# Kernel tuning notes

Measured on AMD Instinct MI355X. Metric: run time of the kernel, lower is better.

The kernel has to match this reference:

```python
import jax, jax.numpy as jnp
import numpy as np

N = 32768      # total nodes
E = 262144     # total edges
B = 32         # graphs in batch
NP = N // B    # nodes per graph (equal-sized graphs)
K = 820        # ceil(0.8 * NP), PyG TopKPooling k
H, C = 8, 64   # heads, per-head channels
NEG_SLOPE = 0.2


def setup_inputs() -> dict:
    key = jax.random.key(0)
    ks = jax.random.split(key, 12)
    s = 0.05
    return {
        "x": jax.random.normal(ks[0], (N, 256), jnp.float32),
        "edge_attr": jax.random.normal(ks[1], (E, 32), jnp.float32),
        "Wl": jax.random.normal(ks[2], (256, H * C), jnp.float32) * s,
        "bl": jax.random.normal(ks[3], (H * C,), jnp.float32) * s,
        "Wr": jax.random.normal(ks[4], (256, H * C), jnp.float32) * s,
        "br": jax.random.normal(ks[5], (H * C,), jnp.float32) * s,
        "We": jax.random.normal(ks[6], (32, H * C), jnp.float32) * s,
        "att": jax.random.normal(ks[7], (H, C), jnp.float32) * s,
        "bias": jax.random.normal(ks[8], (H * C,), jnp.float32) * s,
        "pool_w": jax.random.normal(ks[9], (H * C,), jnp.float32),
        "edge_index": jax.random.randint(ks[10], (2, E), 0, N, jnp.int32),
    }


def reference(x, edge_attr, Wl, bl, Wr, br, We, att, bias, pool_w, edge_index):
    src, dst = edge_index[0], edge_index[1]
    # GATv2Conv (eval mode, dropout off)
    xl = (x @ Wl + bl).reshape(N, H, C)   # x_j side (lin_l)
    xr = (x @ Wr + br).reshape(N, H, C)   # x_i side (lin_r)
    e = (edge_attr @ We).reshape(E, H, C)  # lin_edge, bias=False
    m = jax.nn.leaky_relu(xl[src] + xr[dst] + e, NEG_SLOPE)   # [E,H,C]
    alpha = jnp.einsum('ehc,hc->eh', m, att)                  # [E,H]
    amax = jax.ops.segment_max(alpha, dst, num_segments=N)
    ex = jnp.exp(alpha - amax[dst])
    denom = jax.ops.segment_sum(ex, dst, num_segments=N)
    alpha = ex / denom[dst]                                   # segment softmax over dst
    out = jax.ops.segment_sum(alpha[..., None] * xl[src], dst, num_segments=N)
    h = jax.nn.relu(out.reshape(N, H * C) + bias)             # [N,512]
    # TopKPooling: score = tanh(x.w / ||w||), keep top-k per graph, scale kept rows
    score = jnp.tanh(h @ pool_w / jnp.sqrt(jnp.sum(pool_w * pool_w)))
    vals, idx = jax.lax.top_k(score.reshape(B, NP), K)        # [B,K]
    hg = h.reshape(B, NP, H * C)
    hsel = jnp.take_along_axis(hg, idx[..., None], axis=1) * vals[..., None]  # [B,K,512]
    # global max pool || global mean pool
    gmp = hsel.max(axis=1)
    gap = hsel.mean(axis=1)
    return jnp.concatenate([gmp, gap], axis=1)                # [B,1024]
```

## Files before the change

### kernel.cpp

```cpp
#include <hip/hip_runtime.h>
#include <hip/hip_bf16.h>
#include <cstdint>
#include <cstddef>

#define N_NODES 32768
#define N_EDGES 262144
#define BGRAPH  32
#define NPG     1024
#define KSEL    820
#define NEG     0.2f

typedef unsigned short u16;
typedef __attribute__((ext_vector_type(4))) float f32x4;
typedef __attribute__((ext_vector_type(8))) short s16x8;

static __device__ __forceinline__ u16 f2bf(float v) {
    __hip_bfloat16 b(v);
    return *reinterpret_cast<u16*>(&b);
}
static __device__ __forceinline__ float bf2f(u16 u) {
    __hip_bfloat16 b = *reinterpret_cast<__hip_bfloat16*>(&u);
    return (float)b;
}

__global__ __launch_bounds__(256) void k_split_x(
    const float* __restrict__ x, u16* __restrict__ xhi, u16* __restrict__ xlo)
{
    const int i = blockIdx.x * 256 + threadIdx.x;
    const float4 v = *(const float4*)&x[(size_t)i * 4];
    u16 h0 = f2bf(v.x), h1 = f2bf(v.y), h2 = f2bf(v.z), h3 = f2bf(v.w);
    u16 l0 = f2bf(v.x - bf2f(h0));
    u16 l1 = f2bf(v.y - bf2f(h1));
    u16 l2 = f2bf(v.z - bf2f(h2));
    u16 l3 = f2bf(v.w - bf2f(h3));
    *(ushort4*)&xhi[(size_t)i * 4] = make_ushort4(h0, h1, h2, h3);
    *(ushort4*)&xlo[(size_t)i * 4] = make_ushort4(l0, l1, l2, l3);
}

__global__ __launch_bounds__(256) void k_pack_bt(
    const float* __restrict__ Wl, const float* __restrict__ Wr,
    u16* __restrict__ BpT)
{
    const int kp = blockIdx.x * 256 + threadIdx.x;
    const int n  = blockIdx.y;
    if (kp >= 768) return;
    const float* W = (n < 512) ? Wl : Wr;
    const int col = n & 511;
    const int k = kp & 255;
    const float v = W[(size_t)k * 512 + col];
    const u16 h = f2bf(v);
    const u16 o = (kp >= 256 && kp < 512) ? f2bf(v - bf2f(h)) : h;
    BpT[(size_t)n * 768 + kp] = o;
}

__global__ __launch_bounds__(256) void gemm_mfma(
    const u16* __restrict__ xhi, const u16* __restrict__ xlo,
    const u16* __restrict__ BpT,
    const float* __restrict__ bl, const float* __restrict__ br,
    float* __restrict__ xl, float* __restrict__ xr)
{
    __shared__ u16 As[128 * 64];
    __shared__ u16 Bs[128 * 64];

    const int raw = blockIdx.x;
    const int swz = (raw & 7) * 256 + (raw >> 3);
    const int mt = swz & 255, nt = swz >> 8;
    const int m0 = mt * 128, n0 = nt * 128;

    const int tid  = threadIdx.x;
    const int lane = tid & 63;
    const int wid  = tid >> 6;
    const int wr   = wid >> 1, wc = wid & 1;
    const int lr   = lane & 15;
    const int lk   = lane >> 4;

    f32x4 acc[4][4] = {};

    for (int tk = 0; tk < 12; ++tk) {
        const u16* asrc = (tk < 8) ? xhi : xlo;
        const int  kcol = (tk & 3) * 64;
        __syncthreads();
#pragma unroll
        for (int p = 0; p < 4; ++p) {
            const int c   = tid + p * 256;
            const int row = c >> 3;
            const int ko  = (c & 7) * 8;
            const int di  = row * 64 + (ko ^ ((row & 7) << 3));
            *(uint4*)&As[di] = *(const uint4*)&asrc[(size_t)(m0 + row) * 256 + kcol + ko];
            *(uint4*)&Bs[di] = *(const uint4*)&BpT[(size_t)(n0 + row) * 768 + tk * 64 + ko];
        }
        __syncthreads();
#pragma unroll
        for (int kk = 0; kk < 2; ++kk) {
            s16x8 af[4], bfr[4];
            const int akw = kk * 32 + lk * 8;
#pragma unroll
            for (int i = 0; i < 4; ++i) {
                const int arow = wr * 64 + i * 16 + lr;
                af[i]  = *(const s16x8*)&As[arow * 64 + (akw ^ ((arow & 7) << 3))];
                const int brow = wc * 64 + i * 16 + lr;
                bfr[i] = *(const s16x8*)&Bs[brow * 64 + (akw ^ ((brow & 7) << 3))];
            }
#pragma unroll
            for (int i = 0; i < 4; ++i)
#pragma unroll
                for (int j = 0; j < 4; ++j)
                    acc[i][j] = __builtin_amdgcn_mfma_f32_16x16x32_bf16(
                        af[i], bfr[j], acc[i][j], 0, 0, 0);
        }
    }

    float* const outp = (n0 < 512) ? xl : xr;
    const int ocol0 = n0 & 511;
    const float* const bb = (n0 < 512) ? bl : br;
#pragma unroll
    for (int j = 0; j < 4; ++j) {
        const int col = ocol0 + wc * 64 + j * 16 + lr;
        const float bv = bb[col];
#pragma unroll
        for (int i = 0; i < 4; ++i) {
#pragma unroll
            for (int r = 0; r < 4; ++r) {
                const int rowg = m0 + wr * 64 + i * 16 + (lane >> 4) * 4 + r;
                outp[(size_t)rowg * 512 + col] = acc[i][j][r] + bv;
            }
        }
    }
}

__global__ void k_hist(const int* __restrict__ ei, int* __restrict__ counts)
{
    int e = blockIdx.x * 256 + threadIdx.x;
    if (e < N_EDGES) atomicAdd(&counts[ei[N_EDGES + e]], 1);
}

__global__ __launch_bounds__(1024) void k_scan(
    const int* __restrict__ counts, int* __restrict__ offsets, int* __restrict__ cursors)
{
    __shared__ int part[1024];
    const int tid = threadIdx.x;
    const int base = tid * 32;
    int loc[32];
    int s = 0;
#pragma unroll
    for (int i = 0; i < 32; ++i) { loc[i] = s; s += counts[base + i]; }
    part[tid] = s;
    __syncthreads();
    const int own = s;
    for (int off = 1; off < 1024; off <<= 1) {
        int v = (tid >= off) ? part[tid - off] : 0;
        __syncthreads();
        part[tid] += v;
        __syncthreads();
    }
    const int pre = part[tid] - own;
#pragma unroll
    for (int i = 0; i < 32; ++i) {
        int o = pre + loc[i];
        offsets[base + i] = o;
        cursors[base + i] = o;
    }
}

__global__ void k_scatter(const int* __restrict__ ei, int* __restrict__ cursors,
                          int* __restrict__ sorted_src, int* __restrict__ sorted_dst,
                          int* __restrict__ sorted_eid)
{
    int e = blockIdx.x * 256 + threadIdx.x;
    if (e >= N_EDGES) return;
    int d = ei[N_EDGES + e];
    int pos = atomicAdd(&cursors[d], 1);
    sorted_src[pos] = ei[e];
    sorted_dst[pos] = d;
    sorted_eid[pos] = e;
}

#define EPB 32

__global__ __launch_bounds__(256, 4) void k_alpha(
    const float* __restrict__ xl, const float* __restrict__ xr,
    const float* __restrict__ ea, const float* __restrict__ We,
    const float* __restrict__ att,
    const int* __restrict__ sorted_src, const int* __restrict__ sorted_dst,
    const int* __restrict__ sorted_eid,
    float* __restrict__ logits)
{
    const int tid = threadIdx.x;
    const int c0 = tid * 2;
    const int head = tid >> 5;
    const int lead = ((tid & 31) == 0);

    float2 wr[32];
#pragma unroll
    for (int k = 0; k < 32; ++k)
        wr[k] = *(const float2*)&We[k * 512 + c0];
#pragma unroll
    for (int k = 0; k < 32; ++k)
        asm volatile("" : "+v"(wr[k].x), "+v"(wr[k].y));
    const float2 attv = *(const float2*)&att[c0];

    const int p0 = blockIdx.x * EPB;
    for (int j = 0; j < EPB; j += 2) {
        const int pA = p0 + j, pB = p0 + j + 1;
        const int sA = sorted_src[pA], sB = sorted_src[pB];
        const int dA = sorted_dst[pA], dB = sorted_dst[pB];
        const int eA = sorted_eid[pA], eB = sorted_eid[pB];
        const float2 xlA = *(const float2*)&xl[(size_t)sA * 512 + c0];
        const float2 xrA = *(const float2*)&xr[(size_t)dA * 512 + c0];
        const float2 xlB = *(const float2*)&xl[(size_t)sB * 512 + c0];
        const float2 xrB = *(const float2*)&xr[(size_t)dB * 512 + c0];
        const float* eaA = &ea[(size_t)eA * 32];
        const float* eaB = &ea[(size_t)eB * 32];

        float a0 = 0.f, a1 = 0.f, b0 = 0.f, b1 = 0.f;
#pragma unroll
        for (int k = 0; k < 32; ++k) {
            const float evA = eaA[k];
            const float evB = eaB[k];
            a0 += evA * wr[k].x; a1 += evA * wr[k].y;
            b0 += evB * wr[k].x; b1 += evB * wr[k].y;
        }
        float tA0 = xlA.x + xrA.x + a0; tA0 = tA0 > 0.f ? tA0 : NEG * tA0;
        float tA1 = xlA.y + xrA.y + a1; tA1 = tA1 > 0.f ? tA1 : NEG * tA1;
        float tB0 = xlB.x + xrB.x + b0; tB0 = tB0 > 0.f ? tB0 : NEG * tB0;
        float tB1 = xlB.y + xrB.y + b1; tB1 = tB1 > 0.f ? tB1 : NEG * tB1;

        float lA = tA0 * attv.x + tA1 * attv.y;
        float lB = tB0 * attv.x + tB1 * attv.y;
#pragma unroll
        for (int o = 1; o < 32; o <<= 1) {
            lA += __shfl_xor(lA, o);
            lB += __shfl_xor(lB, o);
        }
        if (lead) {
            logits[(size_t)pA * 8 + head] = lA;
            logits[(size_t)pB * 8 + head] = lB;
        }
    }
}

#define AGG_DPB 8

__global__ __launch_bounds__(256, 8) void k_agg(
    const float* __restrict__ xl, const float* __restrict__ logits,
    const int* __restrict__ sorted_src,
    const int* __restrict__ offsets, const int* __restrict__ counts,
    const float* __restrict__ bias, const float* __restrict__ pw,
    float* __restrict__ h, float* __restrict__ score)
{
    __shared__ float red_s[4];

    const int tid = threadIdx.x;
    const int wv  = tid >> 6;
    const int l   = tid & 63;
    const int c0  = tid * 2;
    const int head = tid >> 5;

    const float2 bv  = *(const float2*)&bias[c0];
    const float2 pwv = *(const float2*)&pw[c0];

    float nrm = pwv.x * pwv.x + pwv.y * pwv.y;
#pragma unroll
    for (int o = 1; o < 64; o <<= 1) nrm += __shfl_xor(nrm, o);
    if (l == 0) red_s[wv] = nrm;
    __syncthreads();
    const float inv_nrm = 1.0f / sqrtf(red_s[0] + red_s[1] + red_s[2] + red_s[3]);

    for (int dd = 0; dd < AGG_DPB; ++dd) {
        const int d   = blockIdx.x * AGG_DPB + dd;
        const int off = offsets[d];
        const int deg = counts[d];

        float m = -INFINITY;
        for (int j = 0; j < deg; ++j)
            m = fmaxf(m, logits[(size_t)(off + j) * 8 + head]);

        float den = 0.f, a0 = 0.f, a1 = 0.f;
        for (int j = 0; j < deg; ++j) {
            const float lg = logits[(size_t)(off + j) * 8 + head];
            const int   s  = sorted_src[off + j];
            const float2 xl2 = *(const float2*)&xl[(size_t)s * 512 + c0];
            const float pe = __expf(lg - m);
            den += pe;
            a0 += pe * xl2.x;
            a1 += pe * xl2.y;
        }

        const float r = den > 0.f ? 1.0f / den : 0.f;
        const float h0 = fmaxf(a0 * r + bv.x, 0.f);
        const float h1 = fmaxf(a1 * r + bv.y, 0.f);
        *(float2*)&h[(size_t)d * 512 + c0] = make_float2(h0, h1);

        float ps = h0 * pwv.x + h1 * pwv.y;
#pragma unroll
        for (int o = 1; o < 64; o <<= 1) ps += __shfl_xor(ps, o);
        __syncthreads();
        if (l == 0) red_s[wv] = ps;
        __syncthreads();
        if (tid == 0)
            score[d] = tanhf((red_s[0] + red_s[1] + red_s[2] + red_s[3]) * inv_nrm);
    }
}

__global__ __launch_bounds__(256) void k_topk(const float* __restrict__ score,
                                              int* __restrict__ sel_idx,
                                              float* __restrict__ sel_val)
{
    __shared__ unsigned long long key[1024];
    const int g = blockIdx.x, tid = threadIdx.x;
    for (int i = tid; i < 1024; i += 256) {
        float s = score[g * 1024 + i];
        unsigned u = __float_as_uint(s);
        u = (u & 0x80000000u) ? ~u : (u | 0x80000000u);
        key[i] = ((unsigned long long)(~u) << 32) | (unsigned)i;
    }
    __syncthreads();
    for (int k = 2; k <= 1024; k <<= 1) {
        for (int j = k >> 1; j > 0; j >>= 1) {
            for (int i = tid; i < 1024; i += 256) {
                int ixj = i ^ j;
                if (ixj > i) {
                    bool up = ((i & k) == 0);
                    unsigned long long a = key[i], b = key[ixj];
                    if ((a > b) == up) { key[i] = b; key[ixj] = a; }
                }
            }
            __syncthreads();
        }
    }
    for (int kk = tid; kk < KSEL; kk += 256) {
        int idx = (int)(key[kk] & 0xFFFFFFFFu);
        sel_idx[g * KSEL + kk] = idx;
        sel_val[g * KSEL + kk] = score[g * 1024 + idx];
    }
}

#define KSLICE 103

__global__ __launch_bounds__(256) void k_pool_part(
    const float* __restrict__ h, const int* __restrict__ sel_idx,
    const float* __restrict__ sel_val, float* __restrict__ part)
{
    const int g = blockIdx.x >> 3, sl = blockIdx.x & 7;
    const int kbeg = sl * KSLICE;
    const int kend = min(KSEL, kbeg + KSLICE);
    const int n = kend - kbeg;
    __shared__ float vs[KSLICE];
    __shared__ int   is_[KSLICE];
    const int tid = threadIdx.x;
    if (tid < n) {
        vs[tid]  = sel_val[g * KSEL + kbeg + tid];
        is_[tid] = sel_idx[g * KSEL + kbeg + tid];
    }
    __syncthreads();
    const int c0 = tid, c1 = tid + 256;
    float mx0 = -INFINITY, mx1 = -INFINITY, s0 = 0.f, s1 = 0.f;
    for (int kk = 0; kk < n; ++kk) {
        const float* hp = h + ((size_t)(g * 1024 + is_[kk])) * 512;
        const float v = vs[kk];
        float f0 = hp[c0] * v, f1 = hp[c1] * v;
        mx0 = fmaxf(mx0, f0); s0 += f0;
        mx1 = fmaxf(mx1, f1); s1 += f1;
    }
    const size_t base = ((size_t)blockIdx.x * 2) * 512;
    part[base + c0] = mx0;        part[base + c1] = mx1;
    part[base + 512 + c0] = s0;   part[base + 512 + c1] = s1;
}

__global__ __launch_bounds__(256) void k_pool_merge(
    const float* __restrict__ part, float* __restrict__ out)
{
    const int g = blockIdx.x, tid = threadIdx.x;
    const int c0 = tid, c1 = tid + 256;
    float mx0 = -INFINITY, mx1 = -INFINITY, s0 = 0.f, s1 = 0.f;
    for (int sl = 0; sl < 8; ++sl) {
        const size_t base = ((size_t)(g * 8 + sl) * 2) * 512;
        mx0 = fmaxf(mx0, part[base + c0]); mx1 = fmaxf(mx1, part[base + c1]);
        s0 += part[base + 512 + c0];       s1 += part[base + 512 + c1];
    }
    out[(size_t)g * 1024 + c0] = mx0;
    out[(size_t)g * 1024 + c1] = mx1;
    out[(size_t)g * 1024 + 512 + c0] = s0 * (1.f / KSEL);
    out[(size_t)g * 1024 + 512 + c1] = s1 * (1.f / KSEL);
}

extern "C" void kernel_launch(void* const* d_in, const int* in_sizes, int n_in,
                              void* d_out, int out_size, void* d_ws, size_t ws_size,
                              hipStream_t stream)
{
    const float* x    = (const float*)d_in[0];
    const float* ea   = (const float*)d_in[1];
    const float* Wl   = (const float*)d_in[2];
    const float* bl   = (const float*)d_in[3];
    const float* Wr   = (const float*)d_in[4];
    const float* br   = (const float*)d_in[5];
    const float* We   = (const float*)d_in[6];
    const float* att  = (const float*)d_in[7];
    const float* bias = (const float*)d_in[8];
    const float* pw   = (const float*)d_in[9];
    const int*   ei   = (const int*)d_in[10];
    float* out = (float*)d_out;

    float* xl        = (float*)d_ws;
    float* xr        = xl + (size_t)N_NODES * 512;
    float* h         = xr + (size_t)N_NODES * 512;
    float* logits    = h + (size_t)N_NODES * 512;
    float* sel_val   = logits + (size_t)N_EDGES * 8;
    float* part      = sel_val + BGRAPH * KSEL;
    float* score     = part + 256 * 2 * 512;
    int* counts      = (int*)(score + N_NODES);
    int* offsets     = counts + N_NODES;
    int* cursors     = offsets + N_NODES;
    int* sorted_src  = cursors + N_NODES;
    int* sorted_dst  = sorted_src + N_EDGES;
    int* sorted_eid  = sorted_dst + N_EDGES;
    int* sel_idx     = sorted_eid + N_EDGES;
    u16* xhi         = (u16*)(sel_idx + BGRAPH * KSEL);
    u16* xlo         = xhi + (size_t)N_NODES * 256;
    u16* bpt         = xlo + (size_t)N_NODES * 256;

    hipMemsetAsync(counts, 0, (size_t)N_NODES * sizeof(int), stream);

    k_split_x<<<(N_NODES * 256) / (4 * 256), 256, 0, stream>>>(x, xhi, xlo);
    k_pack_bt<<<dim3(3, 1024), 256, 0, stream>>>(Wl, Wr, bpt);
    gemm_mfma<<<2048, 256, 0, stream>>>(xhi, xlo, bpt, bl, br, xl, xr);

    k_hist<<<N_EDGES / 256, 256, 0, stream>>>(ei, counts);
    k_scan<<<1, 1024, 0, stream>>>(counts, offsets, cursors);
    k_scatter<<<N_EDGES / 256, 256, 0, stream>>>(ei, cursors, sorted_src, sorted_dst, sorted_eid);
    k_alpha<<<N_EDGES / EPB, 256, 0, stream>>>(xl, xr, ea, We, att,
                                               sorted_src, sorted_dst, sorted_eid, logits);
    k_agg<<<N_NODES / AGG_DPB, 256, 0, stream>>>(xl, logits, sorted_src, offsets, counts,
                                                 bias, pw, h, score);
    k_topk<<<BGRAPH, 256, 0, stream>>>(score, sel_idx, sel_val);
    k_pool_part<<<BGRAPH * 8, 256, 0, stream>>>(h, sel_idx, sel_val, part);
    k_pool_merge<<<BGRAPH, 256, 0, stream>>>(part, out);
}
```

Measured before the change: 679.7 us.

## Compute edge logits with split-bf16 MFMA and use direct global-to-LDS loads in GEMM

The edge-logit kernel is rewritten to compute the edge_attr @ We projection on MFMA units with hi/lo bf16 splitting (three-term product), tiling 64 edges per step and splitting the 512 channels across 4 column slabs in grid.y. The leaky-relu and attention dot product are then fused per slab and reduced with shuffles. Separately, the main GEMM's tile loads now use global_load_lds to write straight into LDS with a pre-swizzled source column, bypassing registers. Risks: slab splitting re-gathers xl/xr rows with less coalescing (16-float runs), and the hi/lo approximation changes precision slightly.

```diff
diff --git a/kernel.cpp b/kernel.cpp
--- a/kernel.cpp
+++ b/kernel.cpp
@@ -21,6 +21,12 @@
 static __device__ __forceinline__ float bf2f(u16 u) {
     __hip_bfloat16 b = *reinterpret_cast<__hip_bfloat16*>(&u);
     return (float)b;
+}
+
+typedef const __attribute__((address_space(1))) void* gas_p;
+typedef __attribute__((address_space(3))) void* las_p;
+static __device__ __forceinline__ void gload16(const void* g, void* l) {
+    __builtin_amdgcn_global_load_lds((gas_p)g, (las_p)l, 16, 0, 0);
 }
 
 __global__ __launch_bounds__(256) void k_split_x(
@@ -82,12 +88,13 @@
         __syncthreads();
 #pragma unroll
         for (int p = 0; p < 4; ++p) {
-            const int c   = tid + p * 256;
+            const int c   = p * 256 + wid * 64 + lane;
             const int row = c >> 3;
-            const int ko  = (c & 7) * 8;
-            const int di  = row * 64 + (ko ^ ((row & 7) << 3));
-            *(uint4*)&As[di] = *(const uint4*)&asrc[(size_t)(m0 + row) * 256 + kcol + ko];
-            *(uint4*)&Bs[di] = *(const uint4*)&BpT[(size_t)(n0 + row) * 768 + tk * 64 + ko];
+            const int cs  = ((c & 7) ^ (row & 7)) * 8;
+            gload16(&asrc[(size_t)(m0 + row) * 256 + kcol + cs],
+                    &As[(size_t)(p * 256 + wid * 64) * 8]);
+            gload16(&BpT[(size_t)(n0 + row) * 768 + tk * 64 + cs],
+                    &Bs[(size_t)(p * 256 + wid * 64) * 8]);
         }
         __syncthreads();
 #pragma unroll
@@ -175,9 +182,9 @@
     sorted_eid[pos] = e;
 }
 
-#define EPB 32
-
-__global__ __launch_bounds__(256, 4) void k_alpha(
+#define LT_TILES 8
+
+__global__ __launch_bounds__(256, 4) void k_logit(
     const float* __restrict__ xl, const float* __restrict__ xr,
     const float* __restrict__ ea, const float* __restrict__ We,
     const float* __restrict__ att,
@@ -185,56 +192,89 @@
     const int* __restrict__ sorted_eid,
     float* __restrict__ logits)
 {
-    const int tid = threadIdx.x;
-    const int c0 = tid * 2;
-    const int head = tid >> 5;
-    const int lead = ((tid & 31) == 0);
-
-    float2 wr[32];
-#pragma unroll
-    for (int k = 0; k < 32; ++k)
-        wr[k] = *(const float2*)&We[k * 512 + c0];
-#pragma unroll
-    for (int k = 0; k < 32; ++k)
-        asm volatile("" : "+v"(wr[k].x), "+v"(wr[k].y));
-    const float2 attv = *(const float2*)&att[c0];
-
-    const int p0 = blockIdx.x * EPB;
-    for (int j = 0; j < EPB; j += 2) {
-        const int pA = p0 + j, pB = p0 + j + 1;
-        const int sA = sorted_src[pA], sB = sorted_src[pB];
-        const int dA = sorted_dst[pA], dB = sorted_dst[pB];
-        const int eA = sorted_eid[pA], eB = sorted_eid[pB];
-        const float2 xlA = *(const float2*)&xl[(size_t)sA * 512 + c0];
-        const float2 xrA = *(const float2*)&xr[(size_t)dA * 512 + c0];
-        const float2 xlB = *(const float2*)&xl[(size_t)sB * 512 + c0];
-        const float2 xrB = *(const float2*)&xr[(size_t)dB * 512 + c0];
-        const float* eaA = &ea[(size_t)eA * 32];
-        const float* eaB = &ea[(size_t)eB * 32];
-
-        float a0 = 0.f, a1 = 0.f, b0 = 0.f, b1 = 0.f;
-#pragma unroll
-        for (int k = 0; k < 32; ++k) {
-            const float evA = eaA[k];
-            const float evB = eaB[k];
-            a0 += evA * wr[k].x; a1 += evA * wr[k].y;
-            b0 += evB * wr[k].x; b1 += evB * wr[k].y;
-        }
-        float tA0 = xlA.x + xrA.x + a0; tA0 = tA0 > 0.f ? tA0 : NEG * tA0;
-        float tA1 = xlA.y + xrA.y + a1; tA1 = tA1 > 0.f ? tA1 : NEG * tA1;
-        float tB0 = xlB.x + xrB.x + b0; tB0 = tB0 > 0.f ? tB0 : NEG * tB0;
-        float tB1 = xlB.y + xrB.y + b1; tB1 = tB1 > 0.f ? tB1 : NEG * tB1;
-
-        float lA = tA0 * attv.x + tA1 * attv.y;
-        float lB = tB0 * attv.x + tB1 * attv.y;
-#pragma unroll
-        for (int o = 1; o < 32; o <<= 1) {
-            lA += __shfl_xor(lA, o);
-            lB += __shfl_xor(lB, o);
-        }
-        if (lead) {
-            logits[(size_t)pA * 8 + head] = lA;
-            logits[(size_t)pB * 8 + head] = lB;
+    __shared__ u16 Ws[128 * 104];
+    __shared__ u16 Ae[64 * 104];
+    __shared__ int eid_s[64], src_s[64], dst_s[64];
+
+    const int tid  = threadIdx.x;
+    const int lane = tid & 63;
+    const int wid  = tid >> 6;
+    const int slab = blockIdx.y;
+    const int lr   = lane & 15;
+    const int lk   = lane >> 4;
+
+    for (int idx = tid; idx < 128 * 96; idx += 256) {
+        const int ch = idx / 96, kp = idx % 96;
+        const int k = (kp < 32) ? kp : ((kp < 64) ? kp - 32 : kp - 64);
+        const float v = We[(size_t)k * 512 + slab * 128 + ch];
+        const u16 h = f2bf(v);
+        Ws[ch * 104 + kp] = (kp >= 64) ? f2bf(v - bf2f(h)) : h;
+    }
+    float attw[8];
+#pragma unroll
+    for (int f = 0; f < 8; ++f) attw[f] = att[slab * 128 + f * 16 + lr];
+
+    for (int t = 0; t < LT_TILES; ++t) {
+        const int ebase = (blockIdx.x * LT_TILES + t) * 64;
+        __syncthreads();
+        if (tid < 64) {
+            eid_s[tid] = sorted_eid[ebase + tid];
+            src_s[tid] = sorted_src[ebase + tid];
+            dst_s[tid] = sorted_dst[ebase + tid];
+        }
+        __syncthreads();
+        for (int idx = tid; idx < 64 * 32; idx += 256) {
+            const int r = idx >> 5, k = idx & 31;
+            const float v = ea[(size_t)eid_s[r] * 32 + k];
+            const u16 h = f2bf(v);
+            Ae[r * 104 + k]      = h;
+            Ae[r * 104 + 32 + k] = f2bf(v - bf2f(h));
+            Ae[r * 104 + 64 + k] = h;
+        }
+        __syncthreads();
+
+        f32x4 acc[8] = {};
+#pragma unroll
+        for (int ks = 0; ks < 3; ++ks) {
+            const s16x8 afr = *(const s16x8*)&Ae[(wid * 16 + lr) * 104 + ks * 32 + lk * 8];
+#pragma unroll
+            for (int f = 0; f < 8; ++f) {
+                const s16x8 bfr = *(const s16x8*)&Ws[(f * 16 + lr) * 104 + ks * 32 + lk * 8];
+                acc[f] = __builtin_amdgcn_mfma_f32_16x16x32_bf16(afr, bfr, acc[f], 0, 0, 0);
+            }
+        }
+
+        float p0[4], p1[4];
+#pragma unroll
+        for (int r = 0; r < 4; ++r) { p0[r] = 0.f; p1[r] = 0.f; }
+#pragma unroll
+        for (int r = 0; r < 4; ++r) {
+            const int el = wid * 16 + lk * 4 + r;
+            const size_t sb = (size_t)src_s[el] * 512 + slab * 128 + lr;
+            const size_t db = (size_t)dst_s[el] * 512 + slab * 128 + lr;
+#pragma unroll
+            for (int f = 0; f < 8; ++f) {
+                const float z = acc[f][r] + xl[sb + f * 16] + xr[db + f * 16];
+                const float tt = z > 0.f ? z : NEG * z;
+                if (f < 4) p0[r] += attw[f] * tt;
+                else       p1[r] += attw[f] * tt;
+            }
+        }
+#pragma unroll
+        for (int o = 1; o < 16; o <<= 1) {
+#pragma unroll
+            for (int r = 0; r < 4; ++r) {
+                p0[r] += __shfl_xor(p0[r], o);
+                p1[r] += __shfl_xor(p1[r], o);
+            }
+        }
+        if (lr == 0) {
+#pragma unroll
+            for (int r = 0; r < 4; ++r) {
+                const size_t eg = ebase + wid * 16 + lk * 4 + r;
+                logits[eg * 8 + slab * 2]     = p0[r];
+                logits[eg * 8 + slab * 2 + 1] = p1[r];
+            }
         }
     }
 }
@@ -428,8 +468,8 @@
     k_hist<<<N_EDGES / 256, 256, 0, stream>>>(ei, counts);
     k_scan<<<1, 1024, 0, stream>>>(counts, offsets, cursors);
     k_scatter<<<N_EDGES / 256, 256, 0, stream>>>(ei, cursors, sorted_src, sorted_dst, sorted_eid);
-    k_alpha<<<N_EDGES / EPB, 256, 0, stream>>>(xl, xr, ea, We, att,
-                                               sorted_src, sorted_dst, sorted_eid, logits);
+    k_logit<<<dim3(N_EDGES / 64 / LT_TILES, 4), 256, 0, stream>>>(
+        xl, xr, ea, We, att, sorted_src, sorted_dst, sorted_eid, logits);
     k_agg<<<N_NODES / AGG_DPB, 256, 0, stream>>>(xl, logits, sorted_src, offsets, counts,
                                                  bias, pw, h, score);
     k_topk<<<BGRAPH, 256, 0, stream>>>(score, sel_idx, sel_val);
```

Result: faster. 605.3 us (-10.9%).
